# Performance work log

Hardware: AMD Instinct MI355X
Metric: run time of the kernel (lower is better)

Reference implementation:

```python
import jax, jax.numpy as jnp
import numpy as np

TOD, DOW = 288, 7
INPUT_LEN, OUTPUT_LEN = 12, 12
N_NODES, R_PATCH, LAYERS = 883, 8, 3
D_IN, D_NODE, D_TOD, D_DOW = 64, 32, 32, 32
DIMS = D_IN + D_NODE + D_TOD + D_DOW  # 160
HID = 2 * DIMS
NEG = -1e9  # finite large-negative mask (avoids NaN on fully-masked rows)


def setup_inputs():
    key = jax.random.key(0)
    ks = jax.random.split(key, 16)
    B = 8
    x = jax.random.normal(ks[0], (B, INPUT_LEN, N_NODES, 1), jnp.float32)
    te = jax.random.randint(ks[1], (B, INPUT_LEN, N_NODES, 2), 0, 7, dtype=jnp.int32)
    s = 0.1
    return {
        "x": x,
        "te": te,
        "patch_emb": jax.random.normal(ks[2], (R_PATCH, D_NODE), jnp.float32) * s,
        "node_table": jax.random.normal(ks[3], (N_NODES, D_NODE), jnp.float32) * s,
        "tod_emb": jax.random.normal(ks[4], (TOD, D_TOD), jnp.float32) * s,
        "dow_emb": jax.random.normal(ks[5], (DOW, D_DOW), jnp.float32) * s,
        "conv_W": jax.random.normal(ks[6], (D_IN, 3, INPUT_LEN), jnp.float32) * s,
        "conv_b": jnp.zeros((D_IN,), jnp.float32),
        # 4 layernorms per layer: [iro1, iro2, ier1, ier2]
        "ln_scale": jnp.ones((LAYERS, 4, DIMS), jnp.float32),
        "ln_bias": jnp.zeros((LAYERS, 4, DIMS), jnp.float32),
        # attn: axis1 = [iro, ier]; axis2 = [q, k, v, out], weights stored [in, out]
        "attn_W": jax.random.normal(ks[7], (LAYERS, 2, 4, DIMS, DIMS), jnp.float32) * 0.05,
        "attn_b": jnp.zeros((LAYERS, 2, 4, DIMS), jnp.float32),
        "mlp_W1": jax.random.normal(ks[8], (LAYERS, 2, DIMS, HID), jnp.float32) * 0.05,
        "mlp_b1": jnp.zeros((LAYERS, 2, HID), jnp.float32),
        "mlp_W2": jax.random.normal(ks[9], (LAYERS, 2, HID, DIMS), jnp.float32) * 0.05,
        "mlp_b2": jnp.zeros((LAYERS, 2, DIMS), jnp.float32),
        "out_W": jax.random.normal(ks[10], (OUTPUT_LEN, DIMS), jnp.float32) * 0.05,
        "out_b": jnp.zeros((OUTPUT_LEN,), jnp.float32),
    }


def _layernorm(x, g, b):
    mu = jnp.mean(x, axis=-1, keepdims=True)
    var = jnp.mean(jnp.square(x - mu), axis=-1, keepdims=True)
    return (x - mu) / jnp.sqrt(var + 1e-5) * g + b


def _mha(x, W, b, key_mask):
    # single-head attention (num_heads=1 in PatchID); x: [..., S, D]
    q = x @ W[0] + b[0]
    k = x @ W[1] + b[1]
    v = x @ W[2] + b[2]
    score = jnp.einsum('...sd,...td->...st', q, k) / np.sqrt(x.shape[-1]).astype(np.float32)
    score = jnp.where(key_mask[..., None, :], score, NEG)
    w = jax.nn.softmax(score, axis=-1)
    o = jnp.einsum('...st,...td->...sd', w, v)
    return o @ W[3] + b[3]


def _forward(x, te, patch_emb, node_table, tod_emb, dow_emb, conv_W, conv_b,
             ln_scale, ln_bias, attn_W, attn_b, mlp_W1, mlp_b1, mlp_W2, mlp_b2,
             out_W, out_b):
    N, R = N_NODES, R_PATCH
    # ---- PatchClassifier (router) ----
    logits = node_table @ patch_emb.T                       # [N, R]
    probs = jax.nn.softmax(logits, axis=-1)
    patch_ids = jnp.argmax(probs, axis=-1)                  # [N]
    hard = jax.nn.one_hot(patch_ids, R, dtype=probs.dtype)
    probs_st = hard - jax.lax.stop_gradient(probs) + probs  # straight-through
    node_soft = probs @ patch_emb                           # [N, D_NODE]
    # ---- embedding ----
    B, T_in = x.shape[0], x.shape[1]
    T = T_in // INPUT_LEN  # = 1
    tef = te.astype(x.dtype)
    x1 = jnp.concatenate([x, tef[..., 0:1] / TOD, tef[..., 1:2] / DOW], axis=-1)  # [B,T_in,N,3]
    x1 = x1.reshape(B, T, INPUT_LEN, N, 3)
    feat = jnp.einsum('btlnc,dcl->btnd', x1, conv_W) + conv_b  # patchified conv
    tid = te[:, -T:, :, 0]
    diw = te[:, -T:, :, 1]
    emb = jnp.concatenate([
        feat, tod_emb[tid], dow_emb[diw],
        jnp.broadcast_to(node_soft, (B, T, N, D_NODE)),
    ], axis=-1)                                             # [B,T,N,DIMS]
    # ---- group_by_patch (static P = N upper bound, masked) ----
    onehot = patch_ids[:, None] == jnp.arange(R)[None, :]
    pos = jnp.cumsum(onehot.astype(jnp.int32), axis=0)[jnp.arange(N), patch_ids] - 1
    P = N
    pf = jnp.zeros((B, T, R, P, DIMS), emb.dtype).at[:, :, patch_ids, pos, :].set(emb)
    mask2d = jnp.zeros((R, P), bool).at[patch_ids, pos].set(True)
    km_iro = mask2d[None, None]       # [1,1,R,P] valid-key mask, keys = P axis
    km_ier = mask2d.T[None, None]     # [1,1,P,R] valid-key mask, keys = R axis
    # ---- encoder layers ----
    for l in range(LAYERS):
        # intra-patch attention over P
        xn = _layernorm(pf, ln_scale[l, 0], ln_bias[l, 0])
        pf = pf + _mha(xn, attn_W[l, 0], attn_b[l, 0], km_iro)
        h = _layernorm(pf, ln_scale[l, 1], ln_bias[l, 1])
        pf = pf + (jax.nn.gelu(h @ mlp_W1[l, 0] + mlp_b1[l, 0], approximate=False)
                   @ mlp_W2[l, 0] + mlp_b2[l, 0])
        # inter-patch attention over R
        xt = jnp.swapaxes(pf, 2, 3)  # [B,T,P,R,D]
        xn = _layernorm(xt, ln_scale[l, 2], ln_bias[l, 2])
        xt = xt + _mha(xn, attn_W[l, 1], attn_b[l, 1], km_ier)
        pf = jnp.swapaxes(xt, 2, 3)
        h = _layernorm(pf, ln_scale[l, 3], ln_bias[l, 3])
        pf = pf + (jax.nn.gelu(h @ mlp_W1[l, 1] + mlp_b1[l, 1], approximate=False)
                   @ mlp_W2[l, 1] + mlp_b2[l, 1])
    # ---- ungroup + 1x1 output conv ----
    out_feat = pf[:, :, patch_ids, pos, :]                  # [B,T,N,DIMS]
    pred = jnp.einsum('btnd,od->bont', out_feat, out_W) + out_b[None, :, None, None]
    return pred, probs_st


def reference(x, te, patch_emb, node_table, tod_emb, dow_emb, conv_W, conv_b,
              ln_scale, ln_bias, attn_W, attn_b, mlp_W1, mlp_b1, mlp_W2, mlp_b2,
              out_W, out_b):
    return _forward(x, te, patch_emb, node_table, tod_emb, dow_emb, conv_W, conv_b,
                    ln_scale, ln_bias, attn_W, attn_b, mlp_W1, mlp_b1, mlp_W2,
                    mlp_b2, out_W, out_b)
```

## Files before the change

### kernel.cpp

```cpp
#include <hip/hip_runtime.h>
#include <hip/hip_cooperative_groups.h>
#include <math.h>

#define NNODES 883
#define BB 8
#define DIMS_ 160
#define HID_ 320
#define PBB 1008
#define RMAX2 (BB*PBB)
#define RMAXP (RMAX2+64)
#define GXNUM (RMAX2/16)

typedef __attribute__((ext_vector_type(8))) short short8v;
typedef __attribute__((ext_vector_type(4))) float fx4;
typedef __attribute__((ext_vector_type(4))) unsigned short ushort4v;

__device__ __forceinline__ unsigned short f2bf(float f) {
  unsigned int u = __float_as_uint(f);
  u = (u + 0x7fffu + ((u >> 16) & 1u)) >> 16;
  return (unsigned short)u;
}
__device__ __forceinline__ float bf2f(unsigned short u) {
  return __uint_as_float(((unsigned int)u) << 16);
}
__device__ __forceinline__ float gelu_f(float v) {
  return 0.5f*v*(1.f + erff(v*0.70710678118654752f));
}

__global__ __launch_bounds__(256)
void zero_pf(float4* __restrict__ p, int n4) {
  int i = blockIdx.x*256 + threadIdx.x;
  if (i < n4) p[i] = float4{0.f, 0.f, 0.f, 0.f};
}

__global__ __launch_bounds__(256)
void zero_flags(int* __restrict__ f, int n) {
  int i = blockIdx.x*256 + threadIdx.x;
  if (i < n) f[i] = 0;
}

__global__ __launch_bounds__(1024)
void patch_scan(const float* __restrict__ node_table,
                const float* __restrict__ patch_emb,
                float* __restrict__ probs_st,
                float* __restrict__ nsoft,
                int* __restrict__ pk, int* __restrict__ cnt,
                int* __restrict__ offs) {
  __shared__ float pe[256];
  __shared__ int pid_s[NNODES];
  __shared__ int cnt_s[8], offs_s[8];
  int t = threadIdx.x;
  for (int k = t; k < 256; k += 1024) pe[k] = patch_emb[k];
  if (t < 8) cnt_s[t] = 0;
  __syncthreads();
  int am = -1;
  if (t < NNODES) {
    float nt[32];
#pragma unroll
    for (int j = 0; j < 32; ++j) nt[j] = node_table[t*32 + j];
    float lg[8];
#pragma unroll
    for (int r = 0; r < 8; ++r) {
      float a = 0.f;
#pragma unroll
      for (int j = 0; j < 32; ++j) a += nt[j] * pe[r*32 + j];
      lg[r] = a;
    }
    float m = lg[0];
#pragma unroll
    for (int r = 1; r < 8; ++r) m = fmaxf(m, lg[r]);
    float e[8]; float s = 0.f;
#pragma unroll
    for (int r = 0; r < 8; ++r) { e[r] = expf(lg[r] - m); s += e[r]; }
    float p[8];
#pragma unroll
    for (int r = 0; r < 8; ++r) p[r] = e[r] / s;
    am = 0; float best = p[0];
#pragma unroll
    for (int r = 1; r < 8; ++r) if (p[r] > best) { best = p[r]; am = r; }
    pid_s[t] = am;
    atomicAdd(&cnt_s[am], 1);
#pragma unroll
    for (int r = 0; r < 8; ++r) {
      float hard = (r == am) ? 1.f : 0.f;
      probs_st[t*8 + r] = (hard - p[r]) + p[r];
    }
#pragma unroll
    for (int j = 0; j < 32; ++j) {
      float a = 0.f;
#pragma unroll
      for (int r = 0; r < 8; ++r) a += p[r] * pe[r*32 + j];
      nsoft[t*32 + j] = a;
    }
  }
  __syncthreads();
  if (t == 0) {
    int o = 0;
#pragma unroll
    for (int r = 0; r < 8; ++r) {
      offs_s[r] = o; offs[r] = o; cnt[r] = cnt_s[r];
      o += (cnt_s[r] + 15) & ~15;
    }
  }
  __syncthreads();
  if (t < NNODES) {
    int pos = 0;
    for (int m = 0; m < t; ++m) pos += (pid_s[m] == am) ? 1 : 0;
    pk[t] = offs_s[am] + pos;
  }
}

__global__ __launch_bounds__(160)
void embed_kernel(const float* __restrict__ x, const int* __restrict__ te,
                  const float* __restrict__ convW, const float* __restrict__ convB,
                  const float* __restrict__ tod, const float* __restrict__ dow,
                  const float* __restrict__ nsoft, const int* __restrict__ pk,
                  const float* __restrict__ g, const float* __restrict__ bt,
                  float* __restrict__ pf, unsigned short* __restrict__ xn) {
  int n = blockIdx.x, b = blockIdx.y, t = threadIdx.x;
  __shared__ float xs[3][12];
  __shared__ float rsum[160], rss[160];
  __shared__ float musv[2];
  if (t < 12) {
    int l = t;
    xs[0][l] = x[(b*12 + l)*NNODES + n];
    int base = ((b*12 + l)*NNODES + n)*2;
    xs[1][l] = (float)te[base]     / 288.0f;
    xs[2][l] = (float)te[base + 1] / 7.0f;
  }
  __syncthreads();
  int row = b*PBB + pk[n];
  float val;
  if (t < 64) {
    float a = convB[t];
#pragma unroll
    for (int c = 0; c < 3; ++c)
#pragma unroll
      for (int l = 0; l < 12; ++l)
        a += xs[c][l] * convW[t*36 + c*12 + l];
    val = a;
  } else if (t < 96) {
    int ti = te[((b*12 + 11)*NNODES + n)*2 + 0];
    val = tod[ti*32 + (t - 64)];
  } else if (t < 128) {
    int dw = te[((b*12 + 11)*NNODES + n)*2 + 1];
    val = dow[dw*32 + (t - 96)];
  } else {
    val = nsoft[n*32 + (t - 128)];
  }
  pf[row*DIMS_ + t] = val;
  rsum[t] = val; rss[t] = val*val;
  __syncthreads();
  if (t < 32) {
    float s = 0.f, ss = 0.f;
#pragma unroll
    for (int j = 0; j < 5; ++j) { s += rsum[t + 32*j]; ss += rss[t + 32*j]; }
    s  += __shfl_xor(s, 1, 32);  ss += __shfl_xor(ss, 1, 32);
    s  += __shfl_xor(s, 2, 32);  ss += __shfl_xor(ss, 2, 32);
    s  += __shfl_xor(s, 4, 32);  ss += __shfl_xor(ss, 4, 32);
    s  += __shfl_xor(s, 8, 32);  ss += __shfl_xor(ss, 8, 32);
    s  += __shfl_xor(s, 16, 32); ss += __shfl_xor(ss, 16, 32);
    if (t == 0) {
      float mu = s*(1.f/160.f);
      float var = ss*(1.f/160.f) - mu*mu;
      musv[0] = mu; musv[1] = rsqrtf(var + 1e-5f);
    }
  }
  __syncthreads();
  xn[(size_t)row*DIMS_ + t] = f2bf((val - musv[0])*musv[1]*g[t] + bt[t]);
}

__global__ __launch_bounds__(256)
void cvt_all(const float* __restrict__ attn_W, const float* __restrict__ mlp_W1,
             const float* __restrict__ mlp_W2,
             unsigned short* __restrict__ wt_attn, unsigned short* __restrict__ wt_w1,
             unsigned short* __restrict__ wt_w2) {
  int y = blockIdx.y;
  const float* src; unsigned short* dst; int K, N;
  if (y < 24)      { src = attn_W + (size_t)y*25600;        dst = wt_attn + (size_t)y*25600; K = 160; N = 160; }
  else if (y < 30) { int q = y-24; src = mlp_W1 + (size_t)q*160*320; dst = wt_w1 + (size_t)q*51200; K = 160; N = 320; }
  else             { int q = y-30; src = mlp_W2 + (size_t)q*320*160; dst = wt_w2 + (size_t)q*51200; K = 320; N = 160; }
  int tn = N >> 5, tk = K >> 5;
  int tile = blockIdx.x;
  if (tile >= tn*tk) return;
  int n0 = (tile % tn) << 5, k0 = (tile / tn) << 5;
  __shared__ unsigned short lds[32][33];
  int col = threadIdx.x & 31, rb = threadIdx.x >> 5;
#pragma unroll
  for (int rr = 0; rr < 4; ++rr) {
    int row = rb + 8*rr;
    lds[row][col] = f2bf(src[(size_t)(k0 + row)*N + n0 + col]);
  }
  __syncthreads();
#pragma unroll
  for (int rr = 0; rr < 4; ++rr) {
    int row = rb + 8*rr;
    dst[(size_t)(n0 + row)*K + k0 + col] = lds[col][row];
  }
}

__device__ __forceinline__ void qkv_from_L1(const char* L1,
    const unsigned short* __restrict__ wq, const float* __restrict__ bq,
    unsigned short* __restrict__ qbN, bool transv,
    int row0, int wid, int r15, int kg) {
  constexpr size_t CY = (size_t)(RMAX2 + 16) * DIMS_;
  fx4 accq[4];
#pragma unroll
  for (int u = 0; u < 4; ++u) accq[u] = (fx4){0.f,0.f,0.f,0.f};
#pragma unroll
  for (int t = 0; t < 5; ++t) {
    short8v a4 = *(const short8v*)(const void*)(L1 + r15*384 + ((t*64 + kg*16) ^ ((r15 & 7) << 4)));
#pragma unroll
    for (int u = 0; u < 4; ++u) {
      int n = wid + 8*u;
      if (n < 30) {
        int z = n / 10, nn = n - z*10;
        short8v bfr = *(const short8v*)(const void*)
            (wq + (size_t)z*25600 + (size_t)(nn*16 + r15)*160 + t*32 + kg*8);
        accq[u] = __builtin_amdgcn_mfma_f32_16x16x32_bf16(a4, bfr, accq[u], 0, 0, 0);
      }
    }
  }
#pragma unroll
  for (int u = 0; u < 4; ++u) {
    int n = wid + 8*u;
    if (n >= 30) continue;
    int z = n / 10, nn = n - z*10;
    int col = nn*16 + r15;
    float bv = bq[z*160 + col];
    unsigned short* C = qbN + (size_t)z * CY;
#pragma unroll
    for (int i = 0; i < 4; ++i) {
      int rr = row0 + 4*kg + i;
      unsigned short h = f2bf(accq[u][i] + bv);
      if (transv && z == 2) C[(size_t)col*RMAXP + rr] = h;
      else                  C[(size_t)rr*DIMS_ + col] = h;
    }
  }
}

__global__ __launch_bounds__(512, 4)
void layers_coop(unsigned short* __restrict__ qbA, unsigned short* __restrict__ qbB,
                 const unsigned short* __restrict__ wt_attn,
                 const unsigned short* __restrict__ wt_w1,
                 const unsigned short* __restrict__ wt_w2,
                 const float* __restrict__ attn_b, const float* __restrict__ mlp_b1,
                 const float* __restrict__ mlp_b2,
                 const float* __restrict__ ln_scale, const float* __restrict__ ln_bias,
                 const unsigned short* __restrict__ xn, float* __restrict__ pf,
                 const int* __restrict__ cnt, const int* __restrict__ offs,
                 int* __restrict__ flags) {
  constexpr size_t CY = (size_t)(RMAX2 + 16) * DIMS_;
  __shared__ unsigned short L1s[16*192];
  __shared__ unsigned short L2s[16*320];
  __shared__ float sA[8][16], ssA[8][16];
  __shared__ float Sf[16*256];
  __shared__ unsigned short Pl[16*256];
  __shared__ float Sinv[16];
  __shared__ int cs[8], os[8];
  char* L1 = (char*)L1s; char* L2 = (char*)L2s; char* Pb = (char*)Pl;
  const float scale = 0.07905694150420949f;

  int tid = threadIdx.x;
  int wid = tid >> 6;
  int lane = tid & 63;
  int r15 = lane & 15, kg = lane >> 4;
  int row0 = blockIdx.x * 16;
  if (tid < 8) { cs[tid] = cnt[tid]; os[tid] = offs[tid]; }
  __syncthreads();
  int b = row0 / PBB;
  int local = row0 - b*PBB;
  int r = 7;
#pragma unroll
  for (int rr = 6; rr >= 0; --rr) if (local < os[rr+1]) r = rr;
  int L = cs[r];
  int q0 = local - os[r];
  int bo = b*PBB + os[r];
  int ntP = (wid < 2) ? 2 : 1;
  int ntM = (wid < 4) ? 3 : 2;

  float trunk[2][4];
#pragma unroll
  for (int u = 0; u < 2; ++u)
    if (u < ntP) {
      int col = (wid + 8*u)*16 + r15;
#pragma unroll
      for (int i = 0; i < 4; ++i)
        trunk[u][i] = pf[(size_t)(row0 + 4*kg + i)*DIMS_ + col];
    }

  for (int k = tid; k < 16*DIMS_; k += 512) {
    int row = k / DIMS_, col = k - row*DIMS_;
    int byte = row*384 + ((col*2) ^ ((row & 7) << 4));
    *(unsigned short*)(L1 + byte) = xn[(size_t)(row0 + row)*DIMS_ + col];
  }
  __syncthreads();
  qkv_from_L1(L1, wt_attn, attn_b, qbA, true, row0, wid, r15, kg);
  __threadfence();
  __syncthreads();
  if (tid == 0)
    __hip_atomic_store(&flags[0*GXNUM + (int)blockIdx.x], 1, __ATOMIC_RELEASE, __HIP_MEMORY_SCOPE_AGENT);

  for (int wb = 0; wb < 6; ++wb) {
    bool intra = ((wb & 1) == 0);
    bool hasnext = (wb < 5);
    unsigned short* qbCur = (wb & 1) ? qbB : qbA;
    unsigned short* qbNext = (wb & 1) ? qbA : qbB;
    const unsigned short* qb = qbCur;
    const unsigned short* kb = qbCur + CY;
    const unsigned short* vt = qbCur + 2*CY;
    const unsigned short* wqkv = wt_attn + (size_t)wb*4*25600;
    const float* bbase = attn_b + (size_t)wb*4*DIMS_;
    const unsigned short* wproj = wqkv + 3*25600;
    const float* bproj = bbase + 3*DIMS_;
    const unsigned short* w1 = wt_w1 + (size_t)wb*51200;
    const unsigned short* w2 = wt_w2 + (size_t)wb*51200;
    const float* b1v = mlp_b1 + (size_t)wb*HID_;
    const float* b2v = mlp_b2 + (size_t)wb*DIMS_;
    const float* g1  = ln_scale + (size_t)(2*wb + 1)*DIMS_;
    const float* bt1 = ln_bias  + (size_t)(2*wb + 1)*DIMS_;
    const float* gn  = ln_scale + (size_t)(2*wb + 2)*DIMS_;
    const float* btn = ln_bias  + (size_t)(2*wb + 2)*DIMS_;
    const unsigned short* wqkvN = wt_attn + (size_t)(wb+1)*4*25600;
    const float* bqkvN = attn_b + (size_t)(wb+1)*4*DIMS_;

    {
      const int fbase = wb*GXNUM;
      if (intra) {
        int nkt = (L + 15) >> 4;
        int blk0 = bo >> 4;
        if (tid < nkt) {
          while (__hip_atomic_load(&flags[fbase + blk0 + tid], __ATOMIC_RELAXED, __HIP_MEMORY_SCOPE_AGENT) == 0) {}
        }
      } else {
        if (tid < 8 && q0 < cs[tid]) {
          int dep = (b*PBB + os[tid] + q0) >> 4;
          while (__hip_atomic_load(&flags[fbase + dep], __ATOMIC_RELAXED, __HIP_MEMORY_SCOPE_AGENT) == 0) {}
        }
      }
      __syncthreads();
      __threadfence();
    }

    if (intra) {
      int nkt = (L + 15) >> 4;
      int npv = (L + 31) >> 5;
      short8v qf[5];
      {
        const unsigned short* Qr = qb + (size_t)(row0 + r15)*DIMS_ + kg*8;
#pragma unroll
        for (int kk = 0; kk < 5; ++kk) qf[kk] = *(const short8v*)(const void*)(Qr + kk*32);
      }
#pragma unroll
      for (int u = 0; u < 2; ++u) {
        int t = wid + 8*u;
        if (t < nkt) {
          fx4 a = (fx4){0.f,0.f,0.f,0.f};
          const unsigned short* Kr = kb + (size_t)(bo + t*16 + r15)*DIMS_ + kg*8;
#pragma unroll
          for (int kk = 0; kk < 5; ++kk) {
            short8v kf = *(const short8v*)(const void*)(Kr + kk*32);
            a = __builtin_amdgcn_mfma_f32_16x16x32_bf16(qf[kk], kf, a, 0, 0, 0);
          }
          int j = t*16 + r15;
#pragma unroll
          for (int i = 0; i < 4; ++i)
            Sf[(4*kg + i)*256 + j] = (j < L) ? a[i]*scale : -1e30f;
        }
      }
      __syncthreads();
      {
        int qq = lane >> 5, l32 = lane & 31;
        int row = 2*wid + qq;
        float vals[8];
        float mx = -1e30f;
#pragma unroll
        for (int k = 0; k < 8; ++k) {
          int j = l32 + 32*k;
          float v = (j < L) ? Sf[row*256 + j] : -1e30f;
          vals[k] = v; mx = fmaxf(mx, v);
        }
        mx = fmaxf(mx, __shfl_xor(mx, 1, 32));
        mx = fmaxf(mx, __shfl_xor(mx, 2, 32));
        mx = fmaxf(mx, __shfl_xor(mx, 4, 32));
        mx = fmaxf(mx, __shfl_xor(mx, 8, 32));
        mx = fmaxf(mx, __shfl_xor(mx, 16, 32));
        float sum = 0.f;
#pragma unroll
        for (int k = 0; k < 8; ++k) {
          float e = (vals[k] > -1e29f) ? expf(vals[k] - mx) : 0.f;
          vals[k] = e; sum += e;
        }
        sum += __shfl_xor(sum, 1, 32);
        sum += __shfl_xor(sum, 2, 32);
        sum += __shfl_xor(sum, 4, 32);
        sum += __shfl_xor(sum, 8, 32);
        sum += __shfl_xor(sum, 16, 32);
        if (l32 == 0) Sinv[row] = (sum > 0.f) ? 1.f/sum : 0.f;
#pragma unroll
        for (int k = 0; k < 8; ++k) {
          int j = l32 + 32*k;
          int byte = row*512 + ((j*2) ^ ((row & 7) << 4));
          *(unsigned short*)(Pb + byte) = f2bf(vals[k]);
        }
      }
      __syncthreads();
      fx4 o[2];
#pragma unroll
      for (int u = 0; u < 2; ++u) o[u] = (fx4){0.f,0.f,0.f,0.f};
#pragma unroll
      for (int sS = 0; sS < 8; ++sS) {
        if (sS < npv) {
          short8v pfr = *(const short8v*)(const void*)
              (Pb + r15*512 + ((sS*64 + kg*16) ^ ((r15 & 7) << 4)));
#pragma unroll
          for (int u = 0; u < 2; ++u)
            if (u < ntP) {
              int n = wid + 8*u;
              const unsigned short* Vr = vt + (size_t)(n*16 + r15)*RMAXP + bo + sS*32 + kg*8;
              short8v vf = *(const short8v*)(const void*)Vr;
              o[u] = __builtin_amdgcn_mfma_f32_16x16x32_bf16(pfr, vf, o[u], 0, 0, 0);
            }
        }
      }
      float inv[4];
#pragma unroll
      for (int i = 0; i < 4; ++i) inv[i] = Sinv[4*kg + i];
#pragma unroll
      for (int u = 0; u < 2; ++u)
        if (u < ntP) {
          int n = wid + 8*u;
#pragma unroll
          for (int i = 0; i < 4; ++i) {
            int row = 4*kg + i, d = n*16 + r15;
            int byte = row*384 + ((d*2) ^ ((row & 7) << 4));
            *(unsigned short*)(L1 + byte) = f2bf(o[u][i]*inv[i]);
          }
        }
    } else {
      int qq = lane >> 5, l32 = lane & 31;
      int rowT = 2*wid + qq;
      int p = q0 + rowT;
      bool vq = p < L;
      int j = l32 >> 2, c = l32 & 3;
      int cj = cs[j];
      bool vk = p < cj;
      int keyrow = b*PBB + os[j] + (vk ? p : 0);
      int qrow = row0 + rowT;
      float part = 0.f;
      {
        const unsigned short* qr = qb + (size_t)qrow*DIMS_ + c*40;
        const unsigned short* kr = kb + (size_t)keyrow*DIMS_ + c*40;
#pragma unroll
        for (int dd = 0; dd < 5; ++dd) {
          short8v a8 = *(const short8v*)(const void*)(qr + dd*8);
          short8v b8 = *(const short8v*)(const void*)(kr + dd*8);
#pragma unroll
          for (int u = 0; u < 8; ++u)
            part += bf2f((unsigned short)a8[u]) * bf2f((unsigned short)b8[u]);
        }
      }
      part += __shfl_xor(part, 1, 4);
      part += __shfl_xor(part, 2, 4);
      float sc = (vq && vk) ? part*scale : -1e30f;
      float m = sc;
      m = fmaxf(m, __shfl_xor(m, 4, 32));
      m = fmaxf(m, __shfl_xor(m, 8, 32));
      m = fmaxf(m, __shfl_xor(m, 16, 32));
      float e = (vq && vk) ? expf(sc - m) : 0.f;
      float sum = e;
      sum += __shfl_xor(sum, 4, 32);
      sum += __shfl_xor(sum, 8, 32);
      sum += __shfl_xor(sum, 16, 32);
      float w = (vq && vk && sum > 0.f) ? e/sum : 0.f;
      float o[5];
#pragma unroll
      for (int k = 0; k < 5; ++k) o[k] = 0.f;
      int qbase = qq*32;
#pragma unroll
      for (int jj = 0; jj < 8; ++jj) {
        float wv = __shfl(w, qbase + jj*4);
        int kr2 = __shfl(keyrow, qbase + jj*4);
        if (wv > 0.f) {
          const unsigned short* Vr = vt + (size_t)kr2*DIMS_;
#pragma unroll
          for (int k = 0; k < 5; ++k) o[k] += wv * bf2f(Vr[l32 + 32*k]);
        }
      }
#pragma unroll
      for (int k = 0; k < 5; ++k) {
        int d = l32 + 32*k;
        int byte = rowT*384 + ((d*2) ^ ((rowT & 7) << 4));
        *(unsigned short*)(L1 + byte) = f2bf(vq ? o[k] : 0.f);
      }
    }
    __syncthreads();

    short8v af[5];
#pragma unroll
    for (int t = 0; t < 5; ++t)
      af[t] = *(const short8v*)(const void*)(L1 + r15*384 + ((t*64 + kg*16) ^ ((r15 & 7) << 4)));
    fx4 acc[2];
#pragma unroll
    for (int u = 0; u < 2; ++u) acc[u] = (fx4){0.f,0.f,0.f,0.f};
#pragma unroll
    for (int t = 0; t < 5; ++t)
#pragma unroll
      for (int u = 0; u < 2; ++u)
        if (u < ntP) {
          int n = wid + 8*u;
          short8v bfr = *(const short8v*)(const void*)(wproj + (size_t)(n*16 + r15)*160 + t*32 + kg*8);
          acc[u] = __builtin_amdgcn_mfma_f32_16x16x32_bf16(af[t], bfr, acc[u], 0, 0, 0);
        }

    float sv[4] = {0,0,0,0}, ssv[4] = {0,0,0,0};
#pragma unroll
    for (int u = 0; u < 2; ++u)
      if (u < ntP) {
        int n = wid + 8*u;
        int col = n*16 + r15;
        float bv = bproj[col];
#pragma unroll
        for (int i = 0; i < 4; ++i) {
          float v = trunk[u][i] + acc[u][i] + bv;
          trunk[u][i] = v;
          sv[i] += v; ssv[i] += v*v;
        }
      }
#pragma unroll
    for (int i = 0; i < 4; ++i) {
      sv[i] += __shfl_xor(sv[i], 1, 16); ssv[i] += __shfl_xor(ssv[i], 1, 16);
      sv[i] += __shfl_xor(sv[i], 2, 16); ssv[i] += __shfl_xor(ssv[i], 2, 16);
      sv[i] += __shfl_xor(sv[i], 4, 16); ssv[i] += __shfl_xor(ssv[i], 4, 16);
      sv[i] += __shfl_xor(sv[i], 8, 16); ssv[i] += __shfl_xor(ssv[i], 8, 16);
    }
    if (r15 == 0) {
#pragma unroll
      for (int i = 0; i < 4; ++i) { sA[wid][4*kg+i] = sv[i]; ssA[wid][4*kg+i] = ssv[i]; }
    }
    __syncthreads();
    float mu[4], rs[4];
#pragma unroll
    for (int i = 0; i < 4; ++i) {
      float st = 0.f, sst = 0.f;
#pragma unroll
      for (int w = 0; w < 8; ++w) { st += sA[w][4*kg+i]; sst += ssA[w][4*kg+i]; }
      mu[i] = st*(1.f/160.f);
      float var = sst*(1.f/160.f) - mu[i]*mu[i];
      rs[i] = rsqrtf(var + 1e-5f);
    }
#pragma unroll
    for (int u = 0; u < 2; ++u)
      if (u < ntP) {
        int n = wid + 8*u;
        int col = n*16 + r15;
        float gv = g1[col], bv = bt1[col];
#pragma unroll
        for (int i = 0; i < 4; ++i) {
          int row = 4*kg + i;
          int byte = row*384 + ((col*2) ^ ((row & 7) << 4));
          *(unsigned short*)(L1 + byte) = f2bf((trunk[u][i] - mu[i])*rs[i]*gv + bv);
        }
      }
    __syncthreads();

    fx4 acc2[3];
#pragma unroll
    for (int u = 0; u < 3; ++u) acc2[u] = (fx4){0.f,0.f,0.f,0.f};
#pragma unroll
    for (int t = 0; t < 5; ++t) {
      short8v a2 = *(const short8v*)(const void*)(L1 + r15*384 + ((t*64 + kg*16) ^ ((r15 & 7) << 4)));
#pragma unroll
      for (int u = 0; u < 3; ++u)
        if (u < ntM) {
          int n = wid + 8*u;
          short8v bfr = *(const short8v*)(const void*)(w1 + (size_t)(n*16 + r15)*160 + t*32 + kg*8);
          acc2[u] = __builtin_amdgcn_mfma_f32_16x16x32_bf16(a2, bfr, acc2[u], 0, 0, 0);
        }
    }
#pragma unroll
    for (int u = 0; u < 3; ++u)
      if (u < ntM) {
        int n = wid + 8*u;
        int col = n*16 + r15;
        float bv = b1v[col];
#pragma unroll
        for (int i = 0; i < 4; ++i) {
          float v = gelu_f(acc2[u][i] + bv);
          int row = 4*kg + i;
          int byte = row*640 + ((col*2) ^ ((row & 7) << 4));
          *(unsigned short*)(L2 + byte) = f2bf(v);
        }
      }
    __syncthreads();

    fx4 acc3[2];
#pragma unroll
    for (int u = 0; u < 2; ++u) acc3[u] = (fx4){0.f,0.f,0.f,0.f};
#pragma unroll
    for (int t = 0; t < 10; ++t) {
      short8v a3 = *(const short8v*)(const void*)(L2 + r15*640 + ((t*64 + kg*16) ^ ((r15 & 7) << 4)));
#pragma unroll
      for (int u = 0; u < 2; ++u)
        if (u < ntP) {
          int n = wid + 8*u;
          short8v bfr = *(const short8v*)(const void*)(w2 + (size_t)(n*16 + r15)*320 + t*32 + kg*8);
          acc3[u] = __builtin_amdgcn_mfma_f32_16x16x32_bf16(a3, bfr, acc3[u], 0, 0, 0);
        }
    }
    float sv2[4] = {0,0,0,0}, ssv2[4] = {0,0,0,0};
#pragma unroll
    for (int u = 0; u < 2; ++u)
      if (u < ntP) {
        int n = wid + 8*u;
        int col = n*16 + r15;
        float bv = b2v[col];
#pragma unroll
        for (int i = 0; i < 4; ++i) {
          float v = trunk[u][i] + acc3[u][i] + bv;
          trunk[u][i] = v;
          sv2[i] += v; ssv2[i] += v*v;
        }
      }

    if (hasnext) {
#pragma unroll
      for (int i = 0; i < 4; ++i) {
        sv2[i] += __shfl_xor(sv2[i], 1, 16); ssv2[i] += __shfl_xor(ssv2[i], 1, 16);
        sv2[i] += __shfl_xor(sv2[i], 2, 16); ssv2[i] += __shfl_xor(ssv2[i], 2, 16);
        sv2[i] += __shfl_xor(sv2[i], 4, 16); ssv2[i] += __shfl_xor(ssv2[i], 4, 16);
        sv2[i] += __shfl_xor(sv2[i], 8, 16); ssv2[i] += __shfl_xor(ssv2[i], 8, 16);
      }
      __syncthreads();
      if (r15 == 0) {
#pragma unroll
        for (int i = 0; i < 4; ++i) { sA[wid][4*kg+i] = sv2[i]; ssA[wid][4*kg+i] = ssv2[i]; }
      }
      __syncthreads();
#pragma unroll
      for (int i = 0; i < 4; ++i) {
        float st = 0.f, sst = 0.f;
#pragma unroll
        for (int w = 0; w < 8; ++w) { st += sA[w][4*kg+i]; sst += ssA[w][4*kg+i]; }
        mu[i] = st*(1.f/160.f);
        float var = sst*(1.f/160.f) - mu[i]*mu[i];
        rs[i] = rsqrtf(var + 1e-5f);
      }
#pragma unroll
      for (int u = 0; u < 2; ++u)
        if (u < ntP) {
          int n = wid + 8*u;
          int col = n*16 + r15;
          float gv = gn[col], bv = btn[col];
#pragma unroll
          for (int i = 0; i < 4; ++i) {
            int row = 4*kg + i;
            int byte = row*384 + ((col*2) ^ ((row & 7) << 4));
            *(unsigned short*)(L1 + byte) = f2bf((trunk[u][i] - mu[i])*rs[i]*gv + bv);
          }
        }
      __syncthreads();

      qkv_from_L1(L1, wqkvN, bqkvN, qbNext, (wb & 1) != 0, row0, wid, r15, kg);
      __threadfence();
      __syncthreads();
      if (tid == 0)
        __hip_atomic_store(&flags[(wb+1)*GXNUM + (int)blockIdx.x], 1, __ATOMIC_RELEASE, __HIP_MEMORY_SCOPE_AGENT);
    }
  }

#pragma unroll
  for (int u = 0; u < 2; ++u)
    if (u < ntP) {
      int col = (wid + 8*u)*16 + r15;
#pragma unroll
      for (int i = 0; i < 4; ++i)
        pf[(size_t)(row0 + 4*kg + i)*DIMS_ + col] = trunk[u][i];
    }
}

template<bool INTRA, bool HASNEXT, bool TRANSV_NEXT>
__global__ __launch_bounds__(512)
void fused_layer(const unsigned short* __restrict__ qb,
                 const unsigned short* __restrict__ kb,
                 const unsigned short* __restrict__ vt,
                 const unsigned short* __restrict__ wproj, const float* __restrict__ bproj,
                 const unsigned short* __restrict__ w1, const float* __restrict__ b1v,
                 const unsigned short* __restrict__ w2, const float* __restrict__ b2v,
                 const float* __restrict__ g1, const float* __restrict__ bt1,
                 const float* __restrict__ gn, const float* __restrict__ btn,
                 const unsigned short* __restrict__ wqkvN, const float* __restrict__ bqkvN,
                 float* __restrict__ pf, unsigned short* __restrict__ qbN,
                 const int* __restrict__ cnt, const int* __restrict__ offs) {
  __shared__ unsigned short L1s[16*192];
  __shared__ unsigned short L2s[16*320];
  __shared__ float sA[8][16], ssA[8][16];
  __shared__ float Sf[INTRA ? 16*256 : 1];
  __shared__ unsigned short Pl[INTRA ? 16*256 : 1];
  __shared__ float Sinv[16];
  __shared__ int cs[8], os[8];
  char* L1 = (char*)L1s; char* L2 = (char*)L2s; char* Pb = (char*)Pl;
  const float scale = 0.07905694150420949f;

  int tid = threadIdx.x;
  int wid = tid >> 6;
  int lane = tid & 63;
  int r15 = lane & 15, kg = lane >> 4;
  int row0 = blockIdx.x * 16;
  if (tid < 8) { cs[tid] = cnt[tid]; os[tid] = offs[tid]; }
  __syncthreads();
  int b = row0 / PBB;
  int local = row0 - b*PBB;
  int r = 7;
#pragma unroll
  for (int rr = 6; rr >= 0; --rr) if (local < os[rr+1]) r = rr;
  int L = cs[r];
  int q0 = local - os[r];
  int bo = b*PBB + os[r];
  int ntP = (wid < 2) ? 2 : 1;
  int ntM = (wid < 4) ? 3 : 2;

  if (INTRA) {
    int nkt = (L + 15) >> 4;
    int npv = (L + 31) >> 5;
    short8v qf[5];
    {
      const unsigned short* Qr = qb + (size_t)(row0 + r15)*DIMS_ + kg*8;
#pragma unroll
      for (int kk = 0; kk < 5; ++kk) qf[kk] = *(const short8v*)(const void*)(Qr + kk*32);
    }
#pragma unroll
    for (int u = 0; u < 2; ++u) {
      int t = wid + 8*u;
      if (t < nkt) {
        fx4 a = (fx4){0.f,0.f,0.f,0.f};
        const unsigned short* Kr = kb + (size_t)(bo + t*16 + r15)*DIMS_ + kg*8;
#pragma unroll
        for (int kk = 0; kk < 5; ++kk) {
          short8v kf = *(const short8v*)(const void*)(Kr + kk*32);
          a = __builtin_amdgcn_mfma_f32_16x16x32_bf16(qf[kk], kf, a, 0, 0, 0);
        }
        int j = t*16 + r15;
#pragma unroll
        for (int i = 0; i < 4; ++i)
          Sf[(4*kg + i)*256 + j] = (j < L) ? a[i]*scale : -1e30f;
      }
    }
    __syncthreads();
    {
      int qq = lane >> 5, l32 = lane & 31;
      int row = 2*wid + qq;
      float vals[8];
      float mx = -1e30f;
#pragma unroll
      for (int k = 0; k < 8; ++k) {
        int j = l32 + 32*k;
        float v = (j < L) ? Sf[row*256 + j] : -1e30f;
        vals[k] = v; mx = fmaxf(mx, v);
      }
      mx = fmaxf(mx, __shfl_xor(mx, 1, 32));
      mx = fmaxf(mx, __shfl_xor(mx, 2, 32));
      mx = fmaxf(mx, __shfl_xor(mx, 4, 32));
      mx = fmaxf(mx, __shfl_xor(mx, 8, 32));
      mx = fmaxf(mx, __shfl_xor(mx, 16, 32));
      float sum = 0.f;
#pragma unroll
      for (int k = 0; k < 8; ++k) {
        float e = (vals[k] > -1e29f) ? expf(vals[k] - mx) : 0.f;
        vals[k] = e; sum += e;
      }
      sum += __shfl_xor(sum, 1, 32);
      sum += __shfl_xor(sum, 2, 32);
      sum += __shfl_xor(sum, 4, 32);
      sum += __shfl_xor(sum, 8, 32);
      sum += __shfl_xor(sum, 16, 32);
      if (l32 == 0) Sinv[row] = (sum > 0.f) ? 1.f/sum : 0.f;
#pragma unroll
      for (int k = 0; k < 8; ++k) {
        int j = l32 + 32*k;
        int byte = row*512 + ((j*2) ^ ((row & 7) << 4));
        *(unsigned short*)(Pb + byte) = f2bf(vals[k]);
      }
    }
    __syncthreads();
    fx4 o[2];
#pragma unroll
    for (int u = 0; u < 2; ++u) o[u] = (fx4){0.f,0.f,0.f,0.f};
#pragma unroll
    for (int sS = 0; sS < 8; ++sS) {
      if (sS < npv) {
        short8v pfr = *(const short8v*)(const void*)
            (Pb + r15*512 + ((sS*64 + kg*16) ^ ((r15 & 7) << 4)));
#pragma unroll
        for (int u = 0; u < 2; ++u)
          if (u < ntP) {
            int n = wid + 8*u;
            const unsigned short* Vr = vt + (size_t)(n*16 + r15)*RMAXP + bo + sS*32 + kg*8;
            short8v vf = *(const short8v*)(const void*)Vr;
            o[u] = __builtin_amdgcn_mfma_f32_16x16x32_bf16(pfr, vf, o[u], 0, 0, 0);
          }
      }
    }
    float inv[4];
#pragma unroll
    for (int i = 0; i < 4; ++i) inv[i] = Sinv[4*kg + i];
#pragma unroll
    for (int u = 0; u < 2; ++u)
      if (u < ntP) {
        int n = wid + 8*u;
#pragma unroll
        for (int i = 0; i < 4; ++i) {
          int row = 4*kg + i, d = n*16 + r15;
          int byte = row*384 + ((d*2) ^ ((row & 7) << 4));
          *(unsigned short*)(L1 + byte) = f2bf(o[u][i]*inv[i]);
        }
      }
  } else {
    int qq = lane >> 5, l32 = lane & 31;
    int rowT = 2*wid + qq;
    int p = q0 + rowT;
    bool vq = p < L;
    int j = l32 >> 2, c = l32 & 3;
    int cj = cs[j];
    bool vk = p < cj;
    int keyrow = b*PBB + os[j] + (vk ? p : 0);
    int qrow = row0 + rowT;
    float part = 0.f;
    {
      const unsigned short* qr = qb + (size_t)qrow*DIMS_ + c*40;
      const unsigned short* kr = kb + (size_t)keyrow*DIMS_ + c*40;
#pragma unroll
      for (int dd = 0; dd < 5; ++dd) {
        short8v a8 = *(const short8v*)(const void*)(qr + dd*8);
        short8v b8 = *(const short8v*)(const void*)(kr + dd*8);
#pragma unroll
        for (int u = 0; u < 8; ++u)
          part += bf2f((unsigned short)a8[u]) * bf2f((unsigned short)b8[u]);
      }
    }
    part += __shfl_xor(part, 1, 4);
    part += __shfl_xor(part, 2, 4);
    float sc = (vq && vk) ? part*scale : -1e30f;
    float m = sc;
    m = fmaxf(m, __shfl_xor(m, 4, 32));
    m = fmaxf(m, __shfl_xor(m, 8, 32));
    m = fmaxf(m, __shfl_xor(m, 16, 32));
    float e = (vq && vk) ? expf(sc - m) : 0.f;
    float sum = e;
    sum += __shfl_xor(sum, 4, 32);
    sum += __shfl_xor(sum, 8, 32);
    sum += __shfl_xor(sum, 16, 32);
    float w = (vq && vk && sum > 0.f) ? e/sum : 0.f;
    float o[5];
#pragma unroll
    for (int k = 0; k < 5; ++k) o[k] = 0.f;
    int qbase = qq*32;
#pragma unroll
    for (int jj = 0; jj < 8; ++jj) {
      float wv = __shfl(w, qbase + jj*4);
      int kr2 = __shfl(keyrow, qbase + jj*4);
      if (wv > 0.f) {
        const unsigned short* Vr = vt + (size_t)kr2*DIMS_;
#pragma unroll
        for (int k = 0; k < 5; ++k) o[k] += wv * bf2f(Vr[l32 + 32*k]);
      }
    }
#pragma unroll
    for (int k = 0; k < 5; ++k) {
      int d = l32 + 32*k;
      int byte = rowT*384 + ((d*2) ^ ((rowT & 7) << 4));
      *(unsigned short*)(L1 + byte) = f2bf(vq ? o[k] : 0.f);
    }
  }
  __syncthreads();

  short8v af[5];
#pragma unroll
  for (int t = 0; t < 5; ++t)
    af[t] = *(const short8v*)(const void*)(L1 + r15*384 + ((t*64 + kg*16) ^ ((r15 & 7) << 4)));
  fx4 acc[2];
#pragma unroll
  for (int u = 0; u < 2; ++u) acc[u] = (fx4){0.f,0.f,0.f,0.f};
#pragma unroll
  for (int t = 0; t < 5; ++t)
#pragma unroll
    for (int u = 0; u < 2; ++u)
      if (u < ntP) {
        int n = wid + 8*u;
        short8v bfr = *(const short8v*)(const void*)(wproj + (size_t)(n*16 + r15)*160 + t*32 + kg*8);
        acc[u] = __builtin_amdgcn_mfma_f32_16x16x32_bf16(af[t], bfr, acc[u], 0, 0, 0);
      }

  float pn[2][4];
  float sv[4] = {0,0,0,0}, ssv[4] = {0,0,0,0};
#pragma unroll
  for (int u = 0; u < 2; ++u)
    if (u < ntP) {
      int n = wid + 8*u;
      int col = n*16 + r15;
      float bv = bproj[col];
#pragma unroll
      for (int i = 0; i < 4; ++i) {
        int row = row0 + 4*kg + i;
        float v = pf[(size_t)row*DIMS_ + col] + acc[u][i] + bv;
        pn[u][i] = v;
        pf[(size_t)row*DIMS_ + col] = v;
        sv[i] += v; ssv[i] += v*v;
      }
    }
#pragma unroll
  for (int i = 0; i < 4; ++i) {
    sv[i] += __shfl_xor(sv[i], 1, 16); ssv[i] += __shfl_xor(ssv[i], 1, 16);
    sv[i] += __shfl_xor(sv[i], 2, 16); ssv[i] += __shfl_xor(ssv[i], 2, 16);
    sv[i] += __shfl_xor(sv[i], 4, 16); ssv[i] += __shfl_xor(ssv[i], 4, 16);
    sv[i] += __shfl_xor(sv[i], 8, 16); ssv[i] += __shfl_xor(ssv[i], 8, 16);
  }
  if (r15 == 0) {
#pragma unroll
    for (int i = 0; i < 4; ++i) { sA[wid][4*kg+i] = sv[i]; ssA[wid][4*kg+i] = ssv[i]; }
  }
  __syncthreads();
  float mu[4], rs[4];
#pragma unroll
  for (int i = 0; i < 4; ++i) {
    float st = 0.f, sst = 0.f;
#pragma unroll
    for (int w = 0; w < 8; ++w) { st += sA[w][4*kg+i]; sst += ssA[w][4*kg+i]; }
    mu[i] = st*(1.f/160.f);
    float var = sst*(1.f/160.f) - mu[i]*mu[i];
    rs[i] = rsqrtf(var + 1e-5f);
  }
#pragma unroll
  for (int u = 0; u < 2; ++u)
    if (u < ntP) {
      int n = wid + 8*u;
      int col = n*16 + r15;
      float gv = g1[col], bv = bt1[col];
#pragma unroll
      for (int i = 0; i < 4; ++i) {
        int row = 4*kg + i;
        int byte = row*384 + ((col*2) ^ ((row & 7) << 4));
        *(unsigned short*)(L1 + byte) = f2bf((pn[u][i] - mu[i])*rs[i]*gv + bv);
      }
    }
  __syncthreads();

  fx4 acc2[3];
#pragma unroll
  for (int u = 0; u < 3; ++u) acc2[u] = (fx4){0.f,0.f,0.f,0.f};
#pragma unroll
  for (int t = 0; t < 5; ++t) {
    short8v a2 = *(const short8v*)(const void*)(L1 + r15*384 + ((t*64 + kg*16) ^ ((r15 & 7) << 4)));
#pragma unroll
    for (int u = 0; u < 3; ++u)
      if (u < ntM) {
        int n = wid + 8*u;
        short8v bfr = *(const short8v*)(const void*)(w1 + (size_t)(n*16 + r15)*160 + t*32 + kg*8);
        acc2[u] = __builtin_amdgcn_mfma_f32_16x16x32_bf16(a2, bfr, acc2[u], 0, 0, 0);
      }
  }
#pragma unroll
  for (int u = 0; u < 3; ++u)
    if (u < ntM) {
      int n = wid + 8*u;
      int col = n*16 + r15;
      float bv = b1v[col];
#pragma unroll
      for (int i = 0; i < 4; ++i) {
        float v = gelu_f(acc2[u][i] + bv);
        int row = 4*kg + i;
        int byte = row*640 + ((col*2) ^ ((row & 7) << 4));
        *(unsigned short*)(L2 + byte) = f2bf(v);
      }
    }
  __syncthreads();

  fx4 acc3[2];
#pragma unroll
  for (int u = 0; u < 2; ++u) acc3[u] = (fx4){0.f,0.f,0.f,0.f};
#pragma unroll
  for (int t = 0; t < 10; ++t) {
    short8v a3 = *(const short8v*)(const void*)(L2 + r15*640 + ((t*64 + kg*16) ^ ((r15 & 7) << 4)));
#pragma unroll
    for (int u = 0; u < 2; ++u)
      if (u < ntP) {
        int n = wid + 8*u;
        short8v bfr = *(const short8v*)(const void*)(w2 + (size_t)(n*16 + r15)*320 + t*32 + kg*8);
        acc3[u] = __builtin_amdgcn_mfma_f32_16x16x32_bf16(a3, bfr, acc3[u], 0, 0, 0);
      }
  }
  float sv2[4] = {0,0,0,0}, ssv2[4] = {0,0,0,0};
  float fnv[2][4];
#pragma unroll
  for (int u = 0; u < 2; ++u)
    if (u < ntP) {
      int n = wid + 8*u;
      int col = n*16 + r15;
      float bv = b2v[col];
#pragma unroll
      for (int i = 0; i < 4; ++i) {
        float v = pn[u][i] + acc3[u][i] + bv;
        fnv[u][i] = v;
        pf[(size_t)(row0 + 4*kg + i)*DIMS_ + col] = v;
        sv2[i] += v; ssv2[i] += v*v;
      }
    }
  if (!HASNEXT) return;

#pragma unroll
  for (int i = 0; i < 4; ++i) {
    sv2[i] += __shfl_xor(sv2[i], 1, 16); ssv2[i] += __shfl_xor(ssv2[i], 1, 16);
    sv2[i] += __shfl_xor(sv2[i], 2, 16); ssv2[i] += __shfl_xor(ssv2[i], 2, 16);
    sv2[i] += __shfl_xor(sv2[i], 4, 16); ssv2[i] += __shfl_xor(ssv2[i], 4, 16);
    sv2[i] += __shfl_xor(sv2[i], 8, 16); ssv2[i] += __shfl_xor(ssv2[i], 8, 16);
  }
  __syncthreads();
  if (r15 == 0) {
#pragma unroll
    for (int i = 0; i < 4; ++i) { sA[wid][4*kg+i] = sv2[i]; ssA[wid][4*kg+i] = ssv2[i]; }
  }
  __syncthreads();
#pragma unroll
  for (int i = 0; i < 4; ++i) {
    float st = 0.f, sst = 0.f;
#pragma unroll
    for (int w = 0; w < 8; ++w) { st += sA[w][4*kg+i]; sst += ssA[w][4*kg+i]; }
    mu[i] = st*(1.f/160.f);
    float var = sst*(1.f/160.f) - mu[i]*mu[i];
    rs[i] = rsqrtf(var + 1e-5f);
  }
#pragma unroll
  for (int u = 0; u < 2; ++u)
    if (u < ntP) {
      int n = wid + 8*u;
      int col = n*16 + r15;
      float gv = gn[col], bv = btn[col];
#pragma unroll
      for (int i = 0; i < 4; ++i) {
        int row = 4*kg + i;
        int byte = row*384 + ((col*2) ^ ((row & 7) << 4));
        *(unsigned short*)(L1 + byte) = f2bf((fnv[u][i] - mu[i])*rs[i]*gv + bv);
      }
    }
  __syncthreads();

  qkv_from_L1(L1, wqkvN, bqkvN, qbN, TRANSV_NEXT, row0, wid, r15, kg);
}

__global__ __launch_bounds__(512)
void qkv0_kernel(const unsigned short* __restrict__ xn,
                 const unsigned short* __restrict__ wt_attn, const float* __restrict__ attn_b,
                 unsigned short* __restrict__ qbA) {
  __shared__ unsigned short L1s[16*192];
  char* L1 = (char*)L1s;
  int tid = threadIdx.x;
  int wid = tid >> 6, lane = tid & 63;
  int r15 = lane & 15, kg = lane >> 4;
  int row0 = blockIdx.x * 16;
  for (int k = tid; k < 16*DIMS_; k += 512) {
    int row = k / DIMS_, col = k - row*DIMS_;
    int byte = row*384 + ((col*2) ^ ((row & 7) << 4));
    *(unsigned short*)(L1 + byte) = xn[(size_t)(row0 + row)*DIMS_ + col];
  }
  __syncthreads();
  qkv_from_L1(L1, wt_attn, attn_b, qbA, true, row0, wid, r15, kg);
}

__global__ __launch_bounds__(256)
void out_kernel(const float* __restrict__ pf, const float* __restrict__ outW,
                const float* __restrict__ outB, const int* __restrict__ pk,
                float* __restrict__ out) {
  int idx = blockIdx.x*256 + threadIdx.x;
  if (idx >= BB*12*NNODES) return;
  int n = idx % NNODES;
  int rest = idx / NNODES;
  int o = rest % 12;
  int b = rest / 12;
  int row = b*PBB + pk[n];
  const float4* Pr = (const float4*)&pf[(size_t)row*DIMS_];
  const float4* Wr = (const float4*)&outW[o*DIMS_];
  float ax=0.f, ay=0.f, az=0.f, aw=0.f;
#pragma unroll
  for (int d4 = 0; d4 < 40; ++d4) {
    float4 a = Pr[d4], c = Wr[d4];
    ax += a.x*c.x; ay += a.y*c.y; az += a.z*c.z; aw += a.w*c.w;
  }
  out[idx] = (ax+ay+az+aw) + outB[o];
}

extern "C" void kernel_launch(void* const* d_in, const int* in_sizes, int n_in,
                              void* d_out, int out_size, void* d_ws, size_t ws_size,
                              hipStream_t stream) {
  const float* x         = (const float*)d_in[0];
  const int*   te        = (const int*)d_in[1];
  const float* patch_emb = (const float*)d_in[2];
  const float* node_tab  = (const float*)d_in[3];
  const float* tod_emb   = (const float*)d_in[4];
  const float* dow_emb   = (const float*)d_in[5];
  const float* conv_W    = (const float*)d_in[6];
  const float* conv_b    = (const float*)d_in[7];
  const float* ln_scale  = (const float*)d_in[8];
  const float* ln_bias   = (const float*)d_in[9];
  const float* attn_W    = (const float*)d_in[10];
  const float* attn_b    = (const float*)d_in[11];
  const float* mlp_W1    = (const float*)d_in[12];
  const float* mlp_b1    = (const float*)d_in[13];
  const float* mlp_W2    = (const float*)d_in[14];
  const float* mlp_b2    = (const float*)d_in[15];
  const float* out_W     = (const float*)d_in[16];
  const float* out_b     = (const float*)d_in[17];

  float* out = (float*)d_out;
  float* probs_st = out + BB*12*NNODES;

  const size_t CY = (size_t)(RMAX2 + 16) * DIMS_;
  const size_t QBSZ = 2*CY + (size_t)DIMS_*RMAXP;

  char* W = (char*)d_ws;
  float* pf = (float*)W;                        W += (size_t)(RMAX2 + 16)*DIMS_*4;
  unsigned short* xn = (unsigned short*)W;      W += (size_t)(RMAX2 + 16)*DIMS_*2;
  unsigned short* qbA = (unsigned short*)W;     W += QBSZ*2;
  unsigned short* qbB = (unsigned short*)W;     W += QBSZ*2;
  unsigned short* wt_attn = (unsigned short*)W; W += (size_t)24*160*160*2;
  unsigned short* wt_w1   = (unsigned short*)W; W += (size_t)6*320*160*2;
  unsigned short* wt_w2   = (unsigned short*)W; W += (size_t)6*160*320*2;
  float* nsoft = (float*)W;                     W += (size_t)NNODES*32*4;
  int* flags = (int*)W;                         W += (size_t)6*GXNUM*4;
  int* pk   = (int*)W;
  int* cnt  = pk + NNODES;
  int* offs = cnt + 8;

  {
    int n4 = (RMAX2 + 16) * DIMS_ / 4;
    zero_pf<<<(n4 + 255)/256, 256, 0, stream>>>((float4*)pf, n4);
  }
  zero_flags<<<(6*GXNUM + 255)/256, 256, 0, stream>>>(flags, 6*GXNUM);
  cvt_all<<<dim3(50, 36), 256, 0, stream>>>(attn_W, mlp_W1, mlp_W2, wt_attn, wt_w1, wt_w2);
  patch_scan<<<1, 1024, 0, stream>>>(node_tab, patch_emb, probs_st, nsoft, pk, cnt, offs);
  embed_kernel<<<dim3(NNODES, BB), 160, 0, stream>>>(x, te, conv_W, conv_b, tod_emb, dow_emb,
                                                     nsoft, pk, ln_scale, ln_bias, pf, xn);

  int maxb = 0;
  hipError_t occ = hipOccupancyMaxActiveBlocksPerMultiprocessor(&maxb, (const void*)layers_coop, 512, 0);
  bool coop_ok = (occ == hipSuccess) && (maxb * 256 >= GXNUM);

  if (coop_ok) {
    void* args[] = {(void*)&qbA, (void*)&qbB, (void*)&wt_attn, (void*)&wt_w1, (void*)&wt_w2,
                    (void*)&attn_b, (void*)&mlp_b1, (void*)&mlp_b2,
                    (void*)&ln_scale, (void*)&ln_bias, (void*)&xn, (void*)&pf,
                    (void*)&cnt, (void*)&offs, (void*)&flags};
    hipError_t e = hipLaunchCooperativeKernel((const void*)layers_coop,
                                              dim3(GXNUM), dim3(512), args, 0, stream);
    coop_ok = (e == hipSuccess);
  }

  if (!coop_ok) {
    qkv0_kernel<<<GXNUM, 512, 0, stream>>>(xn, wt_attn, attn_b, qbA);
    for (int wb = 0; wb < 6; ++wb) {
      unsigned short* qbCur = (wb & 1) ? qbB : qbA;
      unsigned short* qbNext = (wb & 1) ? qbA : qbB;
      const unsigned short* wqkv = wt_attn + (size_t)wb*4*25600;
      const float* bbase = attn_b + (size_t)wb*4*DIMS_;
      const unsigned short* wproj = wqkv + 3*25600;
      const float* bproj = bbase + 3*DIMS_;
      const unsigned short* w1 = wt_w1 + (size_t)wb*51200;
      const unsigned short* w2 = wt_w2 + (size_t)wb*51200;
      const float* b1v = mlp_b1 + (size_t)wb*HID_;
      const float* b2v = mlp_b2 + (size_t)wb*DIMS_;
      const float* g1  = ln_scale + (size_t)(2*wb + 1)*DIMS_;
      const float* bt1 = ln_bias  + (size_t)(2*wb + 1)*DIMS_;
      const float* gn  = ln_scale + (size_t)(2*wb + 2)*DIMS_;
      const float* btn = ln_bias  + (size_t)(2*wb + 2)*DIMS_;
      const unsigned short* wqkvN = wt_attn + (size_t)(wb+1)*4*25600;
      const float* bqkvN = attn_b + (size_t)(wb+1)*4*DIMS_;
      if (wb == 5)
        fused_layer<false,false,false><<<GXNUM, 512, 0, stream>>>(
            qbCur, qbCur + CY, qbCur + 2*CY, wproj, bproj, w1, b1v, w2, b2v,
            g1, bt1, nullptr, nullptr, nullptr, nullptr, pf, qbNext, cnt, offs);
      else if ((wb & 1) == 0)
        fused_layer<true,true,false><<<GXNUM, 512, 0, stream>>>(
            qbCur, qbCur + CY, qbCur + 2*CY, wproj, bproj, w1, b1v, w2, b2v,
            g1, bt1, gn, btn, wqkvN, bqkvN, pf, qbNext, cnt, offs);
      else
        fused_layer<false,true,true><<<GXNUM, 512, 0, stream>>>(
            qbCur, qbCur + CY, qbCur + 2*CY, wproj, bproj, w1, b1v, w2, b2v,
            g1, bt1, gn, btn, wqkvN, bqkvN, pf, qbNext, cnt, offs);
    }
  }

  out_kernel<<<(BB*12*NNODES + 255)/256, 256, 0, stream>>>(pf, out_W, out_b, pk, out);
}
```

Baseline: 263.4 us.

## Fuse output projection into cooperative layer kernel and parallelize patch scan

The final 1x1 output conv is folded into the end of the cooperative layers kernel. Each block stages its trunk rows and the output weights in shared memory, then scatters predictions through a new inverse patch-position map. This removes the pf write-back and the separate out_kernel launch. The patch_scan kernel also replaces its O(N^2) serial position count and shared atomics with wave ballot/popcount prefix sums, at the cost of extra shared memory traffic and a scalar dot loop at the kernel tail.

```diff
diff --git a/kernel.cpp b/kernel.cpp
--- a/kernel.cpp
+++ b/kernel.cpp
@@ -45,13 +45,14 @@
                 float* __restrict__ probs_st,
                 float* __restrict__ nsoft,
                 int* __restrict__ pk, int* __restrict__ cnt,
-                int* __restrict__ offs) {
+                int* __restrict__ offs, int* __restrict__ invp) {
   __shared__ float pe[256];
-  __shared__ int pid_s[NNODES];
-  __shared__ int cnt_s[8], offs_s[8];
+  __shared__ int wtot[8][16], woff[8][16];
+  __shared__ int offs_s[8];
   int t = threadIdx.x;
+  int wv = t >> 6, lane = t & 63;
   for (int k = t; k < 256; k += 1024) pe[k] = patch_emb[k];
-  if (t < 8) cnt_s[t] = 0;
+  if (t < PBB) invp[t] = -1;
   __syncthreads();
   int am = -1;
   if (t < NNODES) {
@@ -78,8 +79,6 @@
     am = 0; float best = p[0];
 #pragma unroll
     for (int r = 1; r < 8; ++r) if (p[r] > best) { best = p[r]; am = r; }
-    pid_s[t] = am;
-    atomicAdd(&cnt_s[am], 1);
 #pragma unroll
     for (int r = 0; r < 8; ++r) {
       float hard = (r == am) ? 1.f : 0.f;
@@ -93,20 +92,37 @@
       nsoft[t*32 + j] = a;
     }
   }
+  unsigned long long lt = (lane == 63) ? 0x7fffffffffffffffull : ((1ull << lane) - 1ull);
+  int myprefix = 0;
+#pragma unroll
+  for (int r = 0; r < 8; ++r) {
+    unsigned long long bm = __ballot(am == r);
+    if (lane == 0) wtot[r][wv] = __popcll(bm);
+    if (am == r) myprefix = __popcll(bm & lt);
+  }
+  __syncthreads();
+  if (t < 128) {
+    int r = t >> 4, w0 = t & 15;
+    int s = 0;
+    for (int w = 0; w < w0; ++w) s += wtot[r][w];
+    woff[r][w0] = s;
+  }
   __syncthreads();
   if (t == 0) {
     int o = 0;
 #pragma unroll
     for (int r = 0; r < 8; ++r) {
-      offs_s[r] = o; offs[r] = o; cnt[r] = cnt_s[r];
-      o += (cnt_s[r] + 15) & ~15;
+      int c = woff[r][15] + wtot[r][15];
+      offs_s[r] = o; offs[r] = o; cnt[r] = c;
+      o += (c + 15) & ~15;
     }
   }
   __syncthreads();
   if (t < NNODES) {
-    int pos = 0;
-    for (int m = 0; m < t; ++m) pos += (pid_s[m] == am) ? 1 : 0;
-    pk[t] = offs_s[am] + pos;
+    int pos = woff[am][wv] + myprefix;
+    int pkv = offs_s[am] + pos;
+    pk[t] = pkv;
+    invp[pkv] = t;
   }
 }
 
@@ -249,7 +265,9 @@
                  const float* __restrict__ ln_scale, const float* __restrict__ ln_bias,
                  const unsigned short* __restrict__ xn, float* __restrict__ pf,
                  const int* __restrict__ cnt, const int* __restrict__ offs,
-                 int* __restrict__ flags) {
+                 int* __restrict__ flags, const int* __restrict__ invp,
+                 const float* __restrict__ outW, const float* __restrict__ outB,
+                 float* __restrict__ outp) {
   constexpr size_t CY = (size_t)(RMAX2 + 16) * DIMS_;
   __shared__ unsigned short L1s[16*192];
   __shared__ unsigned short L2s[16*320];
@@ -669,14 +687,34 @@
     }
   }
 
+  __syncthreads();
+  float* So = Sf;
+  float* Wl = (float*)Pl;
 #pragma unroll
   for (int u = 0; u < 2; ++u)
     if (u < ntP) {
       int col = (wid + 8*u)*16 + r15;
 #pragma unroll
       for (int i = 0; i < 4; ++i)
-        pf[(size_t)(row0 + 4*kg + i)*DIMS_ + col] = trunk[u][i];
-    }
+        So[(4*kg + i)*164 + col] = trunk[u][i];
+    }
+  for (int k = tid; k < 12*160; k += 512) {
+    int o = k / 160, d = k - o*160;
+    Wl[o*161 + d] = outW[k];
+  }
+  __syncthreads();
+  if (tid < 192) {
+    int rr = tid / 12, o = tid - rr*12;
+    int n = invp[local + rr];
+    if (n >= 0) {
+      float a = outB[o];
+      const float* Sr = &So[rr*164];
+      const float* Wr = &Wl[o*161];
+#pragma unroll 8
+      for (int d = 0; d < 160; ++d) a += Sr[d]*Wr[d];
+      outp[(size_t)(b*12 + o)*NNODES + n] = a;
+    }
+  }
 }
 
 template<bool INTRA, bool HASNEXT, bool TRANSV_NEXT>
@@ -1126,6 +1164,7 @@
   unsigned short* wt_w2   = (unsigned short*)W; W += (size_t)6*160*320*2;
   float* nsoft = (float*)W;                     W += (size_t)NNODES*32*4;
   int* flags = (int*)W;                         W += (size_t)6*GXNUM*4;
+  int* invp  = (int*)W;                         W += (size_t)PBB*4;
   int* pk   = (int*)W;
   int* cnt  = pk + NNODES;
   int* offs = cnt + 8;
@@ -1136,7 +1175,7 @@
   }
   zero_flags<<<(6*GXNUM + 255)/256, 256, 0, stream>>>(flags, 6*GXNUM);
   cvt_all<<<dim3(50, 36), 256, 0, stream>>>(attn_W, mlp_W1, mlp_W2, wt_attn, wt_w1, wt_w2);
-  patch_scan<<<1, 1024, 0, stream>>>(node_tab, patch_emb, probs_st, nsoft, pk, cnt, offs);
+  patch_scan<<<1, 1024, 0, stream>>>(node_tab, patch_emb, probs_st, nsoft, pk, cnt, offs, invp);
   embed_kernel<<<dim3(NNODES, BB), 160, 0, stream>>>(x, te, conv_W, conv_b, tod_emb, dow_emb,
                                                      nsoft, pk, ln_scale, ln_bias, pf, xn);
 
@@ -1148,7 +1187,8 @@
     void* args[] = {(void*)&qbA, (void*)&qbB, (void*)&wt_attn, (void*)&wt_w1, (void*)&wt_w2,
                     (void*)&attn_b, (void*)&mlp_b1, (void*)&mlp_b2,
                     (void*)&ln_scale, (void*)&ln_bias, (void*)&xn, (void*)&pf,
-                    (void*)&cnt, (void*)&offs, (void*)&flags};
+                    (void*)&cnt, (void*)&offs, (void*)&flags, (void*)&invp,
+                    (void*)&out_W, (void*)&out_b, (void*)&out};
     hipError_t e = hipLaunchCooperativeKernel((const void*)layers_coop,
                                               dim3(GXNUM), dim3(512), args, 0, stream);
     coop_ok = (e == hipSuccess);
@@ -1186,7 +1226,6 @@
             qbCur, qbCur + CY, qbCur + 2*CY, wproj, bproj, w1, b1v, w2, b2v,
             g1, bt1, gn, btn, wqkvN, bqkvN, pf, qbNext, cnt, offs);
     }
-  }
-
-  out_kernel<<<(BB*12*NNODES + 255)/256, 256, 0, stream>>>(pf, out_W, out_b, pk, out);
-}
+    out_kernel<<<(BB*12*NNODES + 255)/256, 256, 0, stream>>>(pf, out_W, out_b, pk, out);
+  }
+}
```

Result: no change. 258.8 us (-1.7%).
